# Kernel tuning notes

Hardware: AMD Instinct MI355X
Metric: run time of the kernel (lower is better)

## Reference

```python
import jax, jax.numpy as jnp
import numpy as np

IN_FEATURES = 4096
NF = 16384  # output channels (GPT-2 Conv1d 'nf')
B, S = 8, 32


def setup_inputs() -> dict:
    key = jax.random.key(0)
    kx, kw, ks, kb = jax.random.split(key, 4)
    x = jax.random.normal(kx, (B, S, IN_FEATURES), dtype=jnp.float32)
    # int8 quantized weight in [-128, 127]
    weight = jax.random.randint(kw, (IN_FEATURES, NF), -128, 128, dtype=jnp.int32).astype(jnp.int8)
    # per-output-channel dequant scale (small positive values, as |w0|max/128)
    scale = (jax.random.uniform(ks, (1, NF), dtype=jnp.float32) * 0.02 + 1e-4)
    bias = jax.random.normal(kb, (NF,), dtype=jnp.float32)
    return {"x": x, "weight": weight, "scale": scale, "bias": bias}


def reference(x, weight, scale, bias):
    # size_out = x.shape[:-1] + (nf,)
    size_out = x.shape[:-1] + (bias.shape[0],)
    x2 = x.reshape(-1, x.shape[-1])                      # [T, in]
    y = jnp.matmul(x2, weight.astype(x.dtype))            # dequant-to-fp then GEMM: [T, nf]
    y = y * scale + bias                                  # per-channel scale, bias add
    return y.reshape(size_out)
```

## Files before the change

### kernel.cpp

```cpp
#include <hip/hip_runtime.h>
#include <stdint.h>


typedef short bf16x8 __attribute__((ext_vector_type(8)));
typedef float f32x16 __attribute__((ext_vector_type(16)));
typedef int   i32x4  __attribute__((ext_vector_type(4)));
typedef int   i32x2  __attribute__((ext_vector_type(2)));
typedef unsigned short u16x4 __attribute__((ext_vector_type(4)));

#define K_DIM 4096
#define N_DIM 16384
#define BK 128
#define BN 64
#define NIT (K_DIM / BK)
#define KSTEPS 256

__device__ __forceinline__ unsigned fbits(float f) {
  union { float f; unsigned u; } c; c.f = f; return c.u;
}
__device__ __forceinline__ unsigned short bf16rne(float f) {
  unsigned u = fbits(f);
  return (unsigned short)((u + 0x7FFFu + ((u >> 16) & 1u)) >> 16);
}

__global__ __launch_bounds__(256) void cvt_x_frag(const float* __restrict__ x,
                                                  unsigned short* __restrict__ xb) {
  int c    = blockIdx.x * 256 + threadIdx.x;
  int lane = c & 63;
  int ks   = (c >> 6) & 255;
  int mt   = c >> 14;
  int row  = mt * 32 + (lane & 31);
  int k0   = ks * 16 + (lane >> 5) * 8;
  const float4* p = (const float4*)(x + row * K_DIM + k0);
  float4 v0 = p[0], v1 = p[1];
  u16x4 o0, o1;
  o0.x = bf16rne(v0.x); o0.y = bf16rne(v0.y); o0.z = bf16rne(v0.z); o0.w = bf16rne(v0.w);
  o1.x = bf16rne(v1.x); o1.y = bf16rne(v1.y); o1.z = bf16rne(v1.z); o1.w = bf16rne(v1.w);
  u16x4* dst = (u16x4*)(xb + (size_t)c * 8);
  dst[0] = o0;
  dst[1] = o1;
}

__global__ __launch_bounds__(512, 2) void gemm_qconv(
    const unsigned short* __restrict__ xb,
    const int* __restrict__ w,
    const float* __restrict__ scale,
    const float* __restrict__ bias,
    float* __restrict__ out) {
  __shared__ i32x4 Blds[2][16 * 64];

  const int tid  = threadIdx.x;
  const int lane = tid & 63;
  const int wave = tid >> 6;
  const int l31  = lane & 31;
  const int half = lane >> 5;
  const int wm   = wave >> 1;
  const int wn   = wave & 1;
  const int n0   = blockIdx.x * BN;

  const int n2 = tid & 31;
  const int k8 = tid >> 5;
  const int sW = k8 >> 1;
  const int hW = k8 & 1;
  const int nnA = n2 * 2, nnB = n2 * 2 + 1;
  const int slotA = ((nnA >> 5) * 8 + sW) * 64 + (hW * 32 + (nnA & 31));
  const int slotB = ((nnB >> 5) * 8 + sW) * 64 + (hW * 32 + (nnB & 31));

  const int* wbase = w + (k8 * 8) * N_DIM + n0 + n2 * 2;

  i32x2 La[8], Lb[8];
#pragma unroll
  for (int i = 0; i < 8; ++i) La[i] = *(const i32x2*)(wbase + i * N_DIM);

  f32x16 acc0 = {};
  f32x16 acc1 = {};

  const bf16x8* afrag0 = (const bf16x8*)(xb + (size_t)((wm * 2 + 0) * KSTEPS) * 64 * 8);
  const bf16x8* afrag1 = (const bf16x8*)(xb + (size_t)((wm * 2 + 1) * KSTEPS) * 64 * 8);

#define ITER_BODY(IT, LCUR, LNEXT, BUFIDX)                                     \
  {                                                                            \
    bf16x8 A0[8], A1[8];                                                       \
    _Pragma("unroll")                                                          \
    for (int s = 0; s < 8; ++s) {                                              \
      A0[s] = afrag0[((IT) * 8 + s) * 64 + lane];                              \
      A1[s] = afrag1[((IT) * 8 + s) * 64 + lane];                              \
    }                                                                          \
    __builtin_amdgcn_sched_barrier(0);        \
    {                                                                          \
      const int itn = ((IT) + 1 < NIT) ? (IT) + 1 : NIT - 1;  \
      const int* wp = wbase + (size_t)itn * (BK * N_DIM);                      \
      _Pragma("unroll")                                                        \
      for (int i = 0; i < 8; ++i) LNEXT[i] = *(const i32x2*)(wp + i * N_DIM);  \
    }                                                                          \
    __builtin_amdgcn_sched_barrier(0);  \
    i32x4 chA, chB;                                                            \
    _Pragma("unroll")                                                          \
    for (int d = 0; d < 4; ++d) {                                              \
      float a0 = (float)LCUR[2 * d].x, a1 = (float)LCUR[2 * d + 1].x;          \
      float b0 = (float)LCUR[2 * d].y, b1 = (float)LCUR[2 * d + 1].y;          \
      chA[d] = (int)__builtin_amdgcn_perm(fbits(a1), fbits(a0), 0x07060302u);  \
      chB[d] = (int)__builtin_amdgcn_perm(fbits(b1), fbits(b0), 0x07060302u);  \
    }                                                                          \
    Blds[BUFIDX][slotA] = chA;                                                 \
    Blds[BUFIDX][slotB] = chB;                                                 \
    asm volatile("s_waitcnt lgkmcnt(0)" ::: "memory");                         \
    __builtin_amdgcn_s_barrier();                                              \
    __builtin_amdgcn_sched_barrier(0);     \
    _Pragma("unroll")                                                          \
    for (int s = 0; s < 8; ++s) {                                              \
      bf16x8 b = *(const bf16x8*)&Blds[BUFIDX][(wn * 8 + s) * 64 + lane];      \
      acc0 = __builtin_amdgcn_mfma_f32_32x32x16_bf16(A0[s], b, acc0, 0, 0, 0); \
      acc1 = __builtin_amdgcn_mfma_f32_32x32x16_bf16(A1[s], b, acc1, 0, 0, 0); \
    }                                                                          \
  }

#pragma unroll 1
  for (int it = 0; it < NIT; it += 2) {
    ITER_BODY(it,     La, Lb, 0)
    ITER_BODY(it + 1, Lb, La, 1)
  }
#undef ITER_BODY

  const int n = n0 + wn * 32 + l31;
  const float sc = scale[n];
  const float bs = bias[n];
#pragma unroll
  for (int r = 0; r < 2; ++r) {
    const f32x16 acc = r ? acc1 : acc0;
#pragma unroll
    for (int g = 0; g < 16; ++g) {
      const int m = wm * 64 + r * 32 + (g & 3) + 8 * (g >> 2) + 4 * half;
      out[m * N_DIM + n] = acc[g] * sc + bs;
    }
  }
}

extern "C" void kernel_launch(void* const* d_in, const int* in_sizes, int n_in,
                              void* d_out, int out_size, void* d_ws, size_t ws_size,
                              hipStream_t stream) {
  const float* x     = (const float*)d_in[0];
  const int*   wgt   = (const int*)d_in[1];
  const float* scale = (const float*)d_in[2];
  const float* bias  = (const float*)d_in[3];
  float* out = (float*)d_out;
  unsigned short* xb = (unsigned short*)d_ws;

  cvt_x_frag<<<512, 256, 0, stream>>>(x, xb);
  gemm_qconv<<<256, 512, 0, stream>>>(xb, wgt, scale, bias, out);
}
```

Measured before the change: 365.1 us.

## Halve N tile to 32 and double grid to 512 blocks with one M-tile per wave

```diff
diff --git a/kernel.cpp b/kernel.cpp
--- a/kernel.cpp
+++ b/kernel.cpp
@@ -11,7 +11,7 @@
 #define K_DIM 4096
 #define N_DIM 16384
 #define BK 128
-#define BN 64
+#define BN 32
 #define NIT (K_DIM / BK)
 #define KSTEPS 256
 
@@ -41,77 +41,78 @@
   dst[1] = o1;
 }
 
-__global__ __launch_bounds__(512, 2) void gemm_qconv(
+__global__ __launch_bounds__(512, 4) void gemm_qconv(
     const unsigned short* __restrict__ xb,
     const int* __restrict__ w,
     const float* __restrict__ scale,
     const float* __restrict__ bias,
     float* __restrict__ out) {
-  __shared__ i32x4 Blds[2][16 * 64];
+  __shared__ i32x4 Blds[2][8 * 64];
 
   const int tid  = threadIdx.x;
   const int lane = tid & 63;
   const int wave = tid >> 6;
   const int l31  = lane & 31;
   const int half = lane >> 5;
-  const int wm   = wave >> 1;
-  const int wn   = wave & 1;
   const int n0   = blockIdx.x * BN;
 
-  const int n2 = tid & 31;
-  const int k8 = tid >> 5;
-  const int sW = k8 >> 1;
-  const int hW = k8 & 1;
+  const int n2 = tid & 15;
+  const int r8 = tid >> 4;
+  const int sW = r8 >> 2;
+  const int hW = (r8 >> 1) & 1;
+  const int q8 = r8 & 1;
   const int nnA = n2 * 2, nnB = n2 * 2 + 1;
-  const int slotA = ((nnA >> 5) * 8 + sW) * 64 + (hW * 32 + (nnA & 31));
-  const int slotB = ((nnB >> 5) * 8 + sW) * 64 + (hW * 32 + (nnB & 31));
+  const int slotA = (sW * 64 + hW * 32 + nnA) * 2 + q8;
+  const int slotB = (sW * 64 + hW * 32 + nnB) * 2 + q8;
 
-  const int* wbase = w + (k8 * 8) * N_DIM + n0 + n2 * 2;
+  const int* wbase = w + (r8 * 4) * N_DIM + n0 + n2 * 2;
 
-  i32x2 La[8], Lb[8];
+  i32x2 La[4], Lb[4];
 #pragma unroll
-  for (int i = 0; i < 8; ++i) La[i] = *(const i32x2*)(wbase + i * N_DIM);
+  for (int i = 0; i < 4; ++i) La[i] = *(const i32x2*)(wbase + i * N_DIM);
 
-  f32x16 acc0 = {};
-  f32x16 acc1 = {};
+  f32x16 acc = {};
 
-  const bf16x8* afrag0 = (const bf16x8*)(xb + (size_t)((wm * 2 + 0) * KSTEPS) * 64 * 8);
-  const bf16x8* afrag1 = (const bf16x8*)(xb + (size_t)((wm * 2 + 1) * KSTEPS) * 64 * 8);
+  const bf16x8* afrag = (const bf16x8*)(xb + (size_t)(wave * KSTEPS) * 64 * 8);
 
 #define ITER_BODY(IT, LCUR, LNEXT, BUFIDX)                                     \
   {                                                                            \
-    bf16x8 A0[8], A1[8];                                                       \
+    bf16x8 A[8];                                                               \
     _Pragma("unroll")                                                          \
     for (int s = 0; s < 8; ++s) {                                              \
-      A0[s] = afrag0[((IT) * 8 + s) * 64 + lane];                              \
-      A1[s] = afrag1[((IT) * 8 + s) * 64 + lane];                              \
+      A[s] = afrag[((IT) * 8 + s) * 64 + lane];                                \
     }                                                                          \
     __builtin_amdgcn_sched_barrier(0);        \
     {                                                                          \
       const int itn = ((IT) + 1 < NIT) ? (IT) + 1 : NIT - 1;  \
       const int* wp = wbase + (size_t)itn * (BK * N_DIM);                      \
       _Pragma("unroll")                                                        \
-      for (int i = 0; i < 8; ++i) LNEXT[i] = *(const i32x2*)(wp + i * N_DIM);  \
+      for (int i = 0; i < 4; ++i) LNEXT[i] = *(const i32x2*)(wp + i * N_DIM);  \
     }                                                                          \
     __builtin_amdgcn_sched_barrier(0);  \
-    i32x4 chA, chB;                                                            \
-    _Pragma("unroll")                                                          \
-    for (int d = 0; d < 4; ++d) {                                              \
-      float a0 = (float)LCUR[2 * d].x, a1 = (float)LCUR[2 * d + 1].x;          \
-      float b0 = (float)LCUR[2 * d].y, b1 = (float)LCUR[2 * d + 1].y;          \
-      chA[d] = (int)__builtin_amdgcn_perm(fbits(a1), fbits(a0), 0x07060302u);  \
-      chB[d] = (int)__builtin_amdgcn_perm(fbits(b1), fbits(b0), 0x07060302u);  \
+    i32x2 chA, chB;                                                            \
+    {                                                                          \
+      float a0 = (float)LCUR[0].x, a1 = (float)LCUR[1].x;                      \
+      float a2 = (float)LCUR[2].x, a3 = (float)LCUR[3].x;                      \
+      float b0 = (float)LCUR[0].y, b1 = (float)LCUR[1].y;                      \
+      float b2 = (float)LCUR[2].y, b3 = (float)LCUR[3].y;                      \
+      chA.x = (int)__builtin_amdgcn_perm(fbits(a1), fbits(a0), 0x07060302u);   \
+      chA.y = (int)__builtin_amdgcn_perm(fbits(a3), fbits(a2), 0x07060302u);   \
+      chB.x = (int)__builtin_amdgcn_perm(fbits(b1), fbits(b0), 0x07060302u);   \
+      chB.y = (int)__builtin_amdgcn_perm(fbits(b3), fbits(b2), 0x07060302u);   \
     }                                                                          \
-    Blds[BUFIDX][slotA] = chA;                                                 \
-    Blds[BUFIDX][slotB] = chB;                                                 \
+    {                                                                          \
+      i32x2* bb = (i32x2*)&Blds[BUFIDX][0];                                    \
+      bb[slotA] = chA;                                                         \
+      bb[slotB] = chB;                                                         \
+    }                                                                          \
     asm volatile("s_waitcnt lgkmcnt(0)" ::: "memory");                         \
     __builtin_amdgcn_s_barrier();                                              \
     __builtin_amdgcn_sched_barrier(0);     \
     _Pragma("unroll")                                                          \
     for (int s = 0; s < 8; ++s) {                                              \
-      bf16x8 b = *(const bf16x8*)&Blds[BUFIDX][(wn * 8 + s) * 64 + lane];      \
-      acc0 = __builtin_amdgcn_mfma_f32_32x32x16_bf16(A0[s], b, acc0, 0, 0, 0); \
-      acc1 = __builtin_amdgcn_mfma_f32_32x32x16_bf16(A1[s], b, acc1, 0, 0, 0); \
+      bf16x8 b = *(const bf16x8*)&Blds[BUFIDX][s * 64 + lane];                 \
+      acc = __builtin_amdgcn_mfma_f32_32x32x16_bf16(A[s], b, acc, 0, 0, 0);    \
     }                                                                          \
   }
 
@@ -122,17 +123,13 @@
   }
 #undef ITER_BODY
 
-  const int n = n0 + wn * 32 + l31;
+  const int n = n0 + l31;
   const float sc = scale[n];
   const float bs = bias[n];
 #pragma unroll
-  for (int r = 0; r < 2; ++r) {
-    const f32x16 acc = r ? acc1 : acc0;
-#pragma unroll
-    for (int g = 0; g < 16; ++g) {
-      const int m = wm * 64 + r * 32 + (g & 3) + 8 * (g >> 2) + 4 * half;
-      out[m * N_DIM + n] = acc[g] * sc + bs;
-    }
+  for (int g = 0; g < 16; ++g) {
+    const int m = wave * 32 + (g & 3) + 8 * (g >> 2) + 4 * half;
+    out[m * N_DIM + n] = acc[g] * sc + bs;
   }
 }
 
@@ -147,5 +144,5 @@
   unsigned short* xb = (unsigned short*)d_ws;
 
   cvt_x_frag<<<512, 256, 0, stream>>>(x, xb);
-  gemm_qconv<<<256, 512, 0, stream>>>(xb, wgt, scale, bias, out);
+  gemm_qconv<<<512, 512, 0, stream>>>(xb, wgt, scale, bias, out);
 }
```

New measurement: 387.8 us. 1.06x slower.
